# Optimization experiments

Hardware: AMD Instinct MI355X
Metric: run time of the kernel (lower is better)

Reference implementation:

```python
import jax, jax.numpy as jnp
import numpy as np

EPS = 1e-12  # F.normalize eps
CLAMP = 30.0
POS_W = 1.0
NEG_W = 1.0
LABEL_SMOOTHING = 0.0


def _l2_normalize(x):
    n = jnp.sqrt(jnp.sum(x * x, axis=-1, keepdims=True))
    return x / jnp.maximum(n, EPS)


def setup_inputs() -> dict:
    key = jax.random.key(0)
    kv, kt = jax.random.split(key)
    B, D = 8192, 512
    video_features = jax.random.normal(kv, (B, D), dtype=jnp.float32)
    text_features = jax.random.normal(kt, (B, D), dtype=jnp.float32)
    log_temp = jnp.asarray(np.log(0.07), dtype=jnp.float32)  # typical CLIP init
    bias = jnp.asarray(-10.0, dtype=jnp.float32)  # bias_init
    return {
        "video_features": video_features,
        "text_features": text_features,
        "log_temp": log_temp,
        "bias": bias,
    }


def reference(video_features, text_features, log_temp, bias):
    v = _l2_normalize(video_features.astype(jnp.float32))  # [B_v, D]
    t = _l2_normalize(text_features.astype(jnp.float32))   # [B_t, D]
    sim = jnp.einsum("vd,td->vt", v, t)                    # [B_v, B_t]
    temp = jnp.exp(log_temp.astype(jnp.float32))
    logits = jnp.clip(sim / temp + bias, -CLAMP, CLAMP)
    B_v, B_t = v.shape[0], t.shape[0]
    m = min(B_v, B_t)
    # diagonal positive labels (pos_mask is None path)
    labels = jnp.zeros((B_v, B_t), jnp.float32).at[jnp.arange(m), jnp.arange(m)].set(1.0)
    if LABEL_SMOOTHING > 0:
        labels = labels * (1 - LABEL_SMOOTHING) + LABEL_SMOOTHING / 2
    weights = jnp.where(labels > 0.5, POS_W, NEG_W).astype(jnp.float32)
    # numerically stable BCE-with-logits, elementwise then weighted mean
    z = logits
    bce = jnp.maximum(z, 0.0) - z * labels + jnp.log1p(jnp.exp(-jnp.abs(z)))
    return jnp.mean(weights * bce)
```

## Files before the change

kernel.cpp:

```cpp
#include <hip/hip_runtime.h>
#include <cstdint>

#define NB 8192
#define ND 512
#define BM 256
#define BN 256
#define BK 32
#define NT (ND / BK)
#define THREADS 512

typedef __bf16 bf16x8 __attribute__((ext_vector_type(8)));
typedef float f32x4 __attribute__((ext_vector_type(4)));

__device__ __forceinline__ unsigned short f2bf(float f) {
    union { float f; uint32_t u; } c; c.f = f;
    return (unsigned short)((c.u + 0x7fffu + ((c.u >> 16) & 1u)) >> 16);
}

__device__ __forceinline__ void load16(const void* g, void* l) {
    __builtin_amdgcn_global_load_lds(
        (void __attribute__((address_space(1)))*)(const_cast<void*>(g)),
        (void __attribute__((address_space(3)))*)(l),
        16, 0, 0);
}

__global__ __launch_bounds__(256) void norm_cast(const float* __restrict__ v,
                                                 const float* __restrict__ t,
                                                 unsigned short* __restrict__ vn,
                                                 unsigned short* __restrict__ tn,
                                                 int ns) {
    const int wave = threadIdx.x >> 6;
    const int lane = threadIdx.x & 63;
    const int row = blockIdx.x * 4 + wave;
    const float* src;
    unsigned short* dst;
    if (row < NB) {
        src = v + (size_t)row * ND;
        dst = vn + (size_t)row * ns;
    } else {
        src = t + (size_t)(row - NB) * ND;
        dst = tn + (size_t)(row - NB) * ns;
    }
    float4 a = ((const float4*)src)[lane * 2];
    float4 b = ((const float4*)src)[lane * 2 + 1];
    float ss = a.x * a.x + a.y * a.y + a.z * a.z + a.w * a.w
             + b.x * b.x + b.y * b.y + b.z * b.z + b.w * b.w;
#pragma unroll
    for (int off = 32; off; off >>= 1) ss += __shfl_xor(ss, off);
    const float sc = 1.0f / fmaxf(sqrtf(ss), 1e-12f);
    union { unsigned short us[8]; uint4 q; } pk;
    pk.us[0] = f2bf(a.x * sc); pk.us[1] = f2bf(a.y * sc);
    pk.us[2] = f2bf(a.z * sc); pk.us[3] = f2bf(a.w * sc);
    pk.us[4] = f2bf(b.x * sc); pk.us[5] = f2bf(b.y * sc);
    pk.us[6] = f2bf(b.z * sc); pk.us[7] = f2bf(b.w * sc);
    ((uint4*)dst)[lane] = pk.q;
}

__global__ __launch_bounds__(THREADS) void gemm_bce(const unsigned short* __restrict__ vn,
                                                    const unsigned short* __restrict__ tn,
                                                    const float* __restrict__ lt,
                                                    const float* __restrict__ bp,
                                                    float* __restrict__ out_sum,
                                                    int ns) {
    __shared__ __align__(16) unsigned short smem[3 * 2 * BM * BK];
    __shared__ float red[8];

    const int tid = threadIdx.x;
    const int lane = tid & 63;
    const int wave = tid >> 6;
    const int wr = wave >> 2;
    const int wc = wave & 3;
    const int lq = lane & 15;
    const int lh = lane >> 4;

    const int m0 = (int)(blockIdx.x >> 5) * BM;
    const int n0 = (int)(blockIdx.x & 31) * BN;

    const int srow = tid >> 2;
    const int schunk = (tid & 3) ^ (srow & 3);
    const unsigned short* a0 = vn + (size_t)(m0 + srow) * ns + schunk * 8;
    const unsigned short* a1 = vn + (size_t)(m0 + 128 + srow) * ns + schunk * 8;
    const unsigned short* b0 = tn + (size_t)(n0 + srow) * ns + schunk * 8;
    const unsigned short* b1 = tn + (size_t)(n0 + 128 + srow) * ns + schunk * 8;

#define STAGE(t, b) do {                                                   \
        const int k0_ = (t) * BK;                                          \
        unsigned short* As_ = smem + (b) * (2 * BM * BK);                  \
        unsigned short* Bs_ = As_ + BM * BK;                               \
        load16(a0 + k0_, As_ + wave * 512);                                \
        load16(a1 + k0_, As_ + 4096 + wave * 512);                         \
        load16(b0 + k0_, Bs_ + wave * 512);                                \
        load16(b1 + k0_, Bs_ + 4096 + wave * 512);                         \
    } while (0)

    const int swz = (lh ^ (lq & 3)) * 8;
    const int aoff = (wr * 128 + lq) * BK + swz;
    const int boff = (wc * 64 + lq) * BK + swz;

    f32x4 acc[8][4];
#pragma unroll
    for (int m = 0; m < 8; ++m)
#pragma unroll
        for (int n = 0; n < 4; ++n)
            acc[m][n] = f32x4{0.f, 0.f, 0.f, 0.f};

    STAGE(0, 0);
    STAGE(1, 1);
    asm volatile("s_waitcnt vmcnt(4)" ::: "memory");
    __builtin_amdgcn_s_barrier();
    __builtin_amdgcn_sched_barrier(0);

#pragma unroll
    for (int t = 0; t < NT; ++t) {
        const unsigned short* As_ = smem + (t % 3) * (2 * BM * BK);
        const unsigned short* Bs_ = As_ + BM * BK;
        bf16x8 af[8], bfr[4];
#pragma unroll
        for (int m = 0; m < 8; ++m)
            af[m] = *(const bf16x8*)(As_ + aoff + m * 512);
#pragma unroll
        for (int n = 0; n < 4; ++n)
            bfr[n] = *(const bf16x8*)(Bs_ + boff + n * 512);

        if (t + 2 < NT) STAGE(t + 2, (t + 2) % 3);

        __builtin_amdgcn_s_setprio(1);
#pragma unroll
        for (int m = 0; m < 8; ++m)
#pragma unroll
            for (int n = 0; n < 4; ++n)
                acc[m][n] = __builtin_amdgcn_mfma_f32_16x16x32_bf16(af[m], bfr[n], acc[m][n], 0, 0, 0);
        __builtin_amdgcn_s_setprio(0);

        if (t < NT - 2) {
            asm volatile("s_waitcnt vmcnt(4)" ::: "memory");
            __builtin_amdgcn_s_barrier();
            __builtin_amdgcn_sched_barrier(0);
        } else if (t == NT - 2) {
            asm volatile("s_waitcnt vmcnt(0)" ::: "memory");
            __builtin_amdgcn_s_barrier();
            __builtin_amdgcn_sched_barrier(0);
        }
    }
#undef STAGE

    const float invtemp = __expf(-lt[0]);
    const float bias = bp[0];
    float local = 0.f;
    const int row_base = m0 + wr * 128 + lh * 4;
    const int col_base = n0 + wc * 64 + lq;
#pragma unroll
    for (int m = 0; m < 8; ++m) {
#pragma unroll
        for (int n = 0; n < 4; ++n) {
#pragma unroll
            for (int r = 0; r < 4; ++r) {
                const float s = acc[m][n][r];
                float z = fminf(fmaxf(fmaf(s, invtemp, bias), -30.f), 30.f);
                const int gr = row_base + m * 16 + r;
                const int gc = col_base + n * 16;
                local += fmaxf(z, 0.f) + __logf(1.0f + __expf(-fabsf(z))) - ((gr == gc) ? z : 0.f);
            }
        }
    }
#pragma unroll
    for (int off = 32; off; off >>= 1) local += __shfl_xor(local, off);
    if (lane == 0) red[wave] = local;
    __syncthreads();
    if (tid == 0) {
        float tot = 0.f;
#pragma unroll
        for (int w = 0; w < 8; ++w) tot += red[w];
        atomicAdd(out_sum, tot * (1.0f / 67108864.0f));
    }
}

extern "C" void kernel_launch(void* const* d_in, const int* in_sizes, int n_in,
                              void* d_out, int out_size, void* d_ws, size_t ws_size,
                              hipStream_t stream) {
    const float* v = (const float*)d_in[0];
    const float* t = (const float*)d_in[1];
    const float* lt = (const float*)d_in[2];
    const float* bp = (const float*)d_in[3];
    float* out = (float*)d_out;

    const size_t need = (size_t)2 * NB * ND * sizeof(unsigned short);
    unsigned short *vn, *tn;
    int ns;
    if (ws_size >= need) {
        vn = (unsigned short*)d_ws;
        tn = vn + (size_t)NB * ND;
        ns = ND;
    } else {
        vn = (unsigned short*)d_in[0];
        tn = (unsigned short*)d_in[1];
        ns = ND * 2;
    }

    hipMemsetAsync(out, 0, sizeof(float), stream);
    hipLaunchKernelGGL(norm_cast, dim3((2 * NB) / 4), dim3(256), 0, stream, v, t, vn, tn, ns);
    hipLaunchKernelGGL(gemm_bce, dim3((NB / BM) * (NB / BN)), dim3(THREADS), 0, stream,
                       vn, tn, lt, bp, out, ns);
}
```

Baseline: 179.7 us.

## Restructure GEMM mainloop into 8-wave ping-pong schedule with BK=64 double buffering

Doubles the K tile to 64 and switches from a 3-stage buffer to 2-stage double buffering. Each K tile is split into four quarter-phases that interleave LDS fragment reads, async global-to-LDS loads and 16 MFMAs per phase, using explicit vmcnt waits and barriers. The wave-to-output mapping changes to interleaved 16-row/16-col strips with an 8-wide XOR swizzle, and the launch bounds now request 2 blocks per CU. The aim is finer overlap of memory and MFMA work with fewer barriers per FLOP. In exchange, the hand-tuned wait counts are fragile and the extra barriers per tile could stall.

```diff
diff --git a/kernel.cpp b/kernel.cpp
--- a/kernel.cpp
+++ b/kernel.cpp
@@ -5,7 +5,7 @@
 #define ND 512
 #define BM 256
 #define BN 256
-#define BK 32
+#define BK 64
 #define NT (ND / BK)
 #define THREADS 512
 
@@ -34,13 +34,8 @@
     const int row = blockIdx.x * 4 + wave;
     const float* src;
     unsigned short* dst;
-    if (row < NB) {
-        src = v + (size_t)row * ND;
-        dst = vn + (size_t)row * ns;
-    } else {
-        src = t + (size_t)(row - NB) * ND;
-        dst = tn + (size_t)(row - NB) * ns;
-    }
+    if (row < NB) { src = v + (size_t)row * ND; dst = vn + (size_t)row * ns; }
+    else { src = t + (size_t)(row - NB) * ND; dst = tn + (size_t)(row - NB) * ns; }
     float4 a = ((const float4*)src)[lane * 2];
     float4 b = ((const float4*)src)[lane * 2 + 1];
     float ss = a.x * a.x + a.y * a.y + a.z * a.z + a.w * a.w
@@ -56,13 +51,13 @@
     ((uint4*)dst)[lane] = pk.q;
 }
 
-__global__ __launch_bounds__(THREADS) void gemm_bce(const unsigned short* __restrict__ vn,
-                                                    const unsigned short* __restrict__ tn,
-                                                    const float* __restrict__ lt,
-                                                    const float* __restrict__ bp,
-                                                    float* __restrict__ out_sum,
-                                                    int ns) {
-    __shared__ __align__(16) unsigned short smem[3 * 2 * BM * BK];
+__global__ __launch_bounds__(THREADS, 2) void gemm_bce(const unsigned short* __restrict__ vn,
+                                                       const unsigned short* __restrict__ tn,
+                                                       const float* __restrict__ lt,
+                                                       const float* __restrict__ bp,
+                                                       float* __restrict__ out_sum,
+                                                       int ns) {
+    __shared__ __align__(16) unsigned short smem[2 * 2 * BM * BK];
     __shared__ float red[8];
 
     const int tid = threadIdx.x;
@@ -76,26 +71,39 @@
     const int m0 = (int)(blockIdx.x >> 5) * BM;
     const int n0 = (int)(blockIdx.x & 31) * BN;
 
-    const int srow = tid >> 2;
-    const int schunk = (tid & 3) ^ (srow & 3);
-    const unsigned short* a0 = vn + (size_t)(m0 + srow) * ns + schunk * 8;
-    const unsigned short* a1 = vn + (size_t)(m0 + 128 + srow) * ns + schunk * 8;
-    const unsigned short* b0 = tn + (size_t)(n0 + srow) * ns + schunk * 8;
-    const unsigned short* b1 = tn + (size_t)(n0 + 128 + srow) * ns + schunk * 8;
-
-#define STAGE(t, b) do {                                                   \
-        const int k0_ = (t) * BK;                                          \
-        unsigned short* As_ = smem + (b) * (2 * BM * BK);                  \
-        unsigned short* Bs_ = As_ + BM * BK;                               \
-        load16(a0 + k0_, As_ + wave * 512);                                \
-        load16(a1 + k0_, As_ + 4096 + wave * 512);                         \
-        load16(b0 + k0_, Bs_ + wave * 512);                                \
-        load16(b1 + k0_, Bs_ + 4096 + wave * 512);                         \
+    const int sr = tid >> 3;
+    const int sc = (tid & 7) ^ (sr & 7);
+    const unsigned short* sA = vn + (size_t)(m0 + sr) * ns + sc * 8;
+    const unsigned short* sB = tn + (size_t)(n0 + sr) * ns + sc * 8;
+
+#define STG_A(B, T, H) do {                                                    \
+        unsigned short* _d = smem + (B) * 32768 + (((H) * 128) + wave * 8) * 64; \
+        load16(sA + (size_t)((H) * 128) * ns + (T) * 64, _d);                  \
+        load16(sA + (size_t)((H) * 128 + 64) * ns + (T) * 64, _d + 4096);      \
     } while (0)
-
-    const int swz = (lh ^ (lq & 3)) * 8;
-    const int aoff = (wr * 128 + lq) * BK + swz;
-    const int boff = (wc * 64 + lq) * BK + swz;
+#define STG_B(B, T, H) do {                                                    \
+        unsigned short* _d = smem + (B) * 32768 + 16384 + (((H) * 128) + wave * 8) * 64; \
+        load16(sB + (size_t)((H) * 128) * ns + (T) * 64, _d);                  \
+        load16(sB + (size_t)((H) * 128 + 64) * ns + (T) * 64, _d + 4096);      \
+    } while (0)
+
+    const int s0 = ((lh ^ (lq & 7)) * 8);
+    const int aro = (wr * 16 + lq) * 64;
+    const int bro = (wc * 16 + lq) * 64;
+#define RD_A(C, M, KS) (*(const bf16x8*)(smem + (C) * 32768 + aro + (M) * 2048 + ((KS) ? (s0 ^ 32) : s0)))
+#define RD_B(C, N, KS) (*(const bf16x8*)(smem + (C) * 32768 + 16384 + bro + (N) * 4096 + ((KS) ? (s0 ^ 32) : s0)))
+
+#define BAR __builtin_amdgcn_s_barrier()
+#define SCB __builtin_amdgcn_sched_barrier(0)
+#define LGK0 asm volatile("s_waitcnt lgkmcnt(0)" ::: "memory")
+#define VM12 asm volatile("s_waitcnt vmcnt(12)" ::: "memory")
+#define VM10 asm volatile("s_waitcnt vmcnt(10)" ::: "memory")
+#define VM8  asm volatile("s_waitcnt vmcnt(8)" ::: "memory")
+#define VM6  asm volatile("s_waitcnt vmcnt(6)" ::: "memory")
+#define VM4  asm volatile("s_waitcnt vmcnt(4)" ::: "memory")
+#define VM2  asm volatile("s_waitcnt vmcnt(2)" ::: "memory")
+#define VM0  asm volatile("s_waitcnt vmcnt(0)" ::: "memory")
+#define VMNONE ((void)0)
 
     f32x4 acc[8][4];
 #pragma unroll
@@ -104,51 +112,63 @@
         for (int n = 0; n < 4; ++n)
             acc[m][n] = f32x4{0.f, 0.f, 0.f, 0.f};
 
-    STAGE(0, 0);
-    STAGE(1, 1);
-    asm volatile("s_waitcnt vmcnt(4)" ::: "memory");
-    __builtin_amdgcn_s_barrier();
-    __builtin_amdgcn_sched_barrier(0);
-
-#pragma unroll
-    for (int t = 0; t < NT; ++t) {
-        const unsigned short* As_ = smem + (t % 3) * (2 * BM * BK);
-        const unsigned short* Bs_ = As_ + BM * BK;
-        bf16x8 af[8], bfr[4];
-#pragma unroll
-        for (int m = 0; m < 8; ++m)
-            af[m] = *(const bf16x8*)(As_ + aoff + m * 512);
-#pragma unroll
-        for (int n = 0; n < 4; ++n)
-            bfr[n] = *(const bf16x8*)(Bs_ + boff + n * 512);
-
-        if (t + 2 < NT) STAGE(t + 2, (t + 2) % 3);
-
-        __builtin_amdgcn_s_setprio(1);
-#pragma unroll
-        for (int m = 0; m < 8; ++m)
-#pragma unroll
-            for (int n = 0; n < 4; ++n)
-                acc[m][n] = __builtin_amdgcn_mfma_f32_16x16x32_bf16(af[m], bfr[n], acc[m][n], 0, 0, 0);
-        __builtin_amdgcn_s_setprio(0);
-
-        if (t < NT - 2) {
-            asm volatile("s_waitcnt vmcnt(4)" ::: "memory");
-            __builtin_amdgcn_s_barrier();
-            __builtin_amdgcn_sched_barrier(0);
-        } else if (t == NT - 2) {
-            asm volatile("s_waitcnt vmcnt(0)" ::: "memory");
-            __builtin_amdgcn_s_barrier();
-            __builtin_amdgcn_sched_barrier(0);
-        }
-    }
-#undef STAGE
+    bf16x8 afr[4][2], bfr[4][2];
+
+#define MFMA16(MB, N0)                                                          \
+    _Pragma("unroll") for (int mm = 0; mm < 4; ++mm)                            \
+    _Pragma("unroll") for (int nn = 0; nn < 2; ++nn)                            \
+    _Pragma("unroll") for (int kk = 0; kk < 2; ++kk)                            \
+        acc[(MB) + mm][(N0) + nn] = __builtin_amdgcn_mfma_f32_16x16x32_bf16(    \
+            afr[mm][kk], bfr[(N0) + nn][kk], acc[(MB) + mm][(N0) + nn], 0, 0, 0)
+
+#define TILE_BODY(T, S123, S4, W1, W2, W4) do {                                 \
+        const int _cb = (T) & 1, _nb = _cb ^ 1;                                 \
+                                               \
+        _Pragma("unroll") for (int mm = 0; mm < 4; ++mm) {                      \
+            afr[mm][0] = RD_A(_cb, mm, 0); afr[mm][1] = RD_A(_cb, mm, 1); }     \
+        _Pragma("unroll") for (int nn = 0; nn < 2; ++nn) {                      \
+            bfr[nn][0] = RD_B(_cb, nn, 0); bfr[nn][1] = RD_B(_cb, nn, 1); }     \
+        if (S123) STG_B(_nb, (T) + 1, 0);                                       \
+        BAR; LGK0; SCB;                                                         \
+        __builtin_amdgcn_s_setprio(1); MFMA16(0, 0);                            \
+        __builtin_amdgcn_s_setprio(0); W1; BAR; SCB;                            \
+                                                         \
+        _Pragma("unroll") for (int nn = 2; nn < 4; ++nn) {                      \
+            bfr[nn][0] = RD_B(_cb, nn, 0); bfr[nn][1] = RD_B(_cb, nn, 1); }     \
+        if (S123) STG_B(_nb, (T) + 1, 1);                                       \
+        BAR; LGK0; SCB;                                                         \
+        __builtin_amdgcn_s_setprio(1); MFMA16(0, 2);                            \
+        __builtin_amdgcn_s_setprio(0); W2; BAR; SCB;                            \
+                                      \
+        _Pragma("unroll") for (int mm = 0; mm < 4; ++mm) {                      \
+            afr[mm][0] = RD_A(_cb, mm + 4, 0); afr[mm][1] = RD_A(_cb, mm + 4, 1); } \
+        if (S123) STG_A(_nb, (T) + 1, 1);                                       \
+        BAR; LGK0; SCB;                                                         \
+        __builtin_amdgcn_s_setprio(1); MFMA16(4, 0);                            \
+        __builtin_amdgcn_s_setprio(0); BAR; SCB;                                \
+                                                \
+        if (S4) STG_A(_cb, (T) + 2, 0);                                         \
+        BAR; SCB;                                                               \
+        __builtin_amdgcn_s_setprio(1); MFMA16(4, 2);                            \
+        __builtin_amdgcn_s_setprio(0); W4; BAR; SCB;                            \
+    } while (0)
+
+    STG_A(0, 0, 0); STG_B(0, 0, 0); STG_B(0, 0, 1); STG_A(0, 0, 1);
+    STG_A(1, 1, 0); STG_B(1, 1, 0); STG_B(1, 1, 1); STG_A(1, 1, 1);
+    VM12; BAR; SCB;
+
+    TILE_BODY(0, false, true, VM10, VM8, VM6);
+    for (int t = 1; t <= 6; ++t) {
+        const bool s4 = (t <= 5);
+        TILE_BODY(t, true, s4, VM6, VM6, VM6);
+    }
+    TILE_BODY(7, false, false, VM2, VM0, VMNONE);
 
     const float invtemp = __expf(-lt[0]);
     const float bias = bp[0];
     float local = 0.f;
-    const int row_base = m0 + wr * 128 + lh * 4;
-    const int col_base = n0 + wc * 64 + lq;
+    const int row_base = m0 + wr * 16 + lh * 4;
+    const int col_base = n0 + wc * 16 + lq;
 #pragma unroll
     for (int m = 0; m < 8; ++m) {
 #pragma unroll
@@ -157,8 +177,8 @@
             for (int r = 0; r < 4; ++r) {
                 const float s = acc[m][n][r];
                 float z = fminf(fmaxf(fmaf(s, invtemp, bias), -30.f), 30.f);
-                const int gr = row_base + m * 16 + r;
-                const int gc = col_base + n * 16;
+                const int gr = row_base + m * 32 + r;
+                const int gc = col_base + n * 64;
                 local += fmaxf(z, 0.f) + __logf(1.0f + __expf(-fabsf(z))) - ((gr == gc) ? z : 0.f);
             }
         }
```

New measurement: 177.5 us. About the same (-1.2%).
